# Kernel optimization log

Measured on AMD Instinct MI355X. Metric: run time of the kernel, lower is better.

## Reference

```python
import jax, jax.numpy as jnp
import numpy as np

ALPHA = 0.2  # LeakyReLU negative slope
N, IN_DIM, OUT_DIM = 8192, 128, 64


def setup_inputs() -> dict:
    key = jax.random.key(0)
    k1, k2, k3, k4 = jax.random.split(key, 4)
    x = jax.random.normal(k1, (N, IN_DIM), dtype=jnp.float32)
    adj = jax.random.randint(k2, (N, N), 0, 2, dtype=jnp.int32)
    W = jax.random.normal(k3, (IN_DIM, OUT_DIM), dtype=jnp.float32) * 0.1
    a = jax.random.normal(k4, (2 * OUT_DIM, 1), dtype=jnp.float32) * 0.1
    return {"x": x, "adj": adj, "W": W, "a": a}


def reference(x, adj, W, a):
    # h = x @ W : [N, out]
    h = x @ W
    # e_ij = LeakyReLU(a^T [h_i || h_j]) computed as broadcast sum of the
    # two halves of the attention vector (avoids materializing [N,N,2*out]).
    a_src = a[:OUT_DIM, 0]   # [out]
    a_dst = a[OUT_DIM:, 0]   # [out]
    e = (h @ a_src)[:, None] + (h @ a_dst)[None, :]      # [N, N]
    e = jnp.where(e > 0, e, ALPHA * e)                    # LeakyReLU
    # mask non-edges, row-softmax
    e = jnp.where(adj > 0, e, jnp.float32(-9e15))
    attn = jax.nn.softmax(e, axis=-1)                     # [N, N]
    out = attn @ h                                        # [N, out]
    # concat=True -> ELU nonlinearity
    return jax.nn.elu(out)
```

## Files before the change

kernel.cpp:

```cpp
#include <hip/hip_runtime.h>
#include <hip/hip_bf16.h>
#include <cstdint>
#include <cstddef>

#define N_NODES 8192
#define IN_DIM  128
#define OUT_DIM 64
#define LRELU_ALPHA 0.2f
#define S_SLICES 4
#define LOG2E 1.44269504f

using f32x16 = __attribute__((ext_vector_type(16))) float;
using bf16x8 = __attribute__((ext_vector_type(8))) short;

typedef const __attribute__((address_space(1))) int* gas_ptr;
typedef __attribute__((address_space(3))) int* las_ptr;

static __device__ __forceinline__ unsigned short f2bf(float x) {
    union { float f; unsigned u; } v; v.f = x;
    unsigned r = v.u + 0x7FFFu + ((v.u >> 16) & 1u);
    return (unsigned short)(r >> 16);
}

__global__ __launch_bounds__(256) void gat_prep(
    const float* __restrict__ x, const float* __restrict__ W,
    const float* __restrict__ a,
    float* __restrict__ svec, float* __restrict__ dvec,
    unsigned short* __restrict__ hpack)
{
    __shared__ float shA[4][8][64];
    const int tid = threadIdx.x;
    const int w   = tid >> 6;
    const int f   = tid & 63;
    const int i0  = blockIdx.x * 8;

    float acc[8];
#pragma unroll
    for (int r = 0; r < 8; ++r) acc[r] = 0.f;

    const int k0 = w * 32;
#pragma unroll 2
    for (int k = k0; k < k0 + 32; k += 4) {
        const float w0 = W[(k + 0) * OUT_DIM + f];
        const float w1 = W[(k + 1) * OUT_DIM + f];
        const float w2 = W[(k + 2) * OUT_DIM + f];
        const float w3 = W[(k + 3) * OUT_DIM + f];
#pragma unroll
        for (int r = 0; r < 8; ++r) {
            const float4 xv = *reinterpret_cast<const float4*>(
                x + (size_t)(i0 + r) * IN_DIM + k);
            acc[r] = fmaf(xv.x, w0, acc[r]);
            acc[r] = fmaf(xv.y, w1, acc[r]);
            acc[r] = fmaf(xv.z, w2, acc[r]);
            acc[r] = fmaf(xv.w, w3, acc[r]);
        }
    }
#pragma unroll
    for (int r = 0; r < 8; ++r) shA[w][r][f] = acc[r];
    __syncthreads();

    if (w == 0) {
        union { unsigned short us[8]; int4 v; } pk;
#pragma unroll
        for (int r = 0; r < 8; ++r) {
            const float hv = shA[0][r][f] + shA[1][r][f] + shA[2][r][f] + shA[3][r][f];
            pk.us[r] = f2bf(hv);
        }
        const int jb    = i0 >> 4;
        const int jhalf = (i0 >> 3) & 1;
        const int fb    = f >> 5;
        const int lidx  = (f & 31) + 32 * jhalf;
        *reinterpret_cast<int4*>(hpack + ((size_t)(jb * 2 + fb) * 64 + lidx) * 8) = pk.v;
    } else if (w == 1) {
        const float asrc = a[f];
#pragma unroll
        for (int r = 0; r < 8; ++r) {
            const float hv = shA[0][r][f] + shA[1][r][f] + shA[2][r][f] + shA[3][r][f];
            float sv = hv * asrc;
#pragma unroll
            for (int off = 32; off >= 1; off >>= 1) sv += __shfl_xor(sv, off);
            if (f == 0) svec[i0 + r] = sv * LOG2E;
        }
    } else if (w == 2) {
        const float adst = a[OUT_DIM + f];
#pragma unroll
        for (int r = 0; r < 8; ++r) {
            const float hv = shA[0][r][f] + shA[1][r][f] + shA[2][r][f] + shA[3][r][f];
            float dv = hv * adst;
#pragma unroll
            for (int off = 32; off >= 1; off >>= 1) dv += __shfl_xor(dv, off);
            if (f == 0) dvec[i0 + r] = dv * LOG2E;
        }
    }
}

__global__ __launch_bounds__(256, 4) void gat_main(
    const int* __restrict__ adj,
    const float* __restrict__ svec, const float* __restrict__ dvec,
    const unsigned short* __restrict__ hpack,
    float* __restrict__ pO, float* __restrict__ pDen)
{
    union SH {
        int tiles[2][32 * 128];
        struct { float red[4][32][64]; float redden[4][32]; } r;
    };
    __shared__ SH sh;

    const int tid = threadIdx.x;
    const int w   = tid >> 6;
    const int l   = tid & 63;
    const int rb  = blockIdx.x;
    const int sl  = blockIdx.y;
    const int row = l & 31;
    const int kh  = l >> 5;
    const int i0  = rb * 32;
    const int jwin = sl * 2048;

    const float s_i = svec[i0 + row];
    asm volatile("" :: "v"(s_i));
    const bf16x8* hp = reinterpret_cast<const bf16x8*>(hpack);

    auto stage = [&](int buf, int ss) {
        const int jt0 = jwin + ss * 128;
#pragma unroll
        for (int q = 0; q < 4; ++q) {
            const int r0   = (w * 4 + q) * 2;
            const int lrow = r0 + (l >> 5);
            const int cp   = l & 31;
            const int cg   = cp ^ (lrow & 7);
            const int* gsrc = adj + (size_t)(i0 + lrow) * N_NODES + jt0 + cg * 4;
            int* ldst = &sh.tiles[buf][r0 * 128];
            __builtin_amdgcn_global_load_lds((gas_ptr)gsrc, (las_ptr)ldst, 16, 0, 0);
        }
    };

    f32x16 acc0, acc1;
#pragma unroll
    for (int r = 0; r < 16; ++r) { acc0[r] = 0.f; acc1[r] = 0.f; }
    float den = 0.f;

    stage(0, 0);
    stage(1, 1);

    const int swz = row & 7;
    for (int s = 0; s < 16; ++s) {
        const int buf = s & 1;
        const int jt0 = jwin + s * 128;
        const int jg  = jt0 + w * 32;
        const int jb  = jg >> 4;

        const bf16x8 b00 = hp[(jb * 2 + 0) * 64 + l];
        const bf16x8 b01 = hp[(jb * 2 + 1) * 64 + l];
        const bf16x8 b10 = hp[(jb * 2 + 2) * 64 + l];
        const bf16x8 b11 = hp[(jb * 2 + 3) * 64 + l];
        const int j0 = jg + kh * 8;
        const float4 dA0 = *reinterpret_cast<const float4*>(dvec + j0);
        const float4 dA1 = *reinterpret_cast<const float4*>(dvec + j0 + 4);
        const float4 dB0 = *reinterpret_cast<const float4*>(dvec + j0 + 16);
        const float4 dB1 = *reinterpret_cast<const float4*>(dvec + j0 + 20);

        asm volatile("s_waitcnt vmcnt(12)" ::: "memory");
        __builtin_amdgcn_s_barrier();

        const int* tb = &sh.tiles[buf][0];
        const int c00 = w * 8 + kh * 2;
        const int c10 = w * 8 + 4 + kh * 2;
        const int4 A00 = *reinterpret_cast<const int4*>(&tb[row * 128 + ((c00    ) ^ swz) * 4]);
        const int4 A01 = *reinterpret_cast<const int4*>(&tb[row * 128 + ((c00 + 1) ^ swz) * 4]);
        const int4 A10 = *reinterpret_cast<const int4*>(&tb[row * 128 + ((c10    ) ^ swz) * 4]);
        const int4 A11 = *reinterpret_cast<const int4*>(&tb[row * 128 + ((c10 + 1) ^ swz) * 4]);
        asm volatile("s_waitcnt lgkmcnt(0)" ::: "memory");
        __builtin_amdgcn_s_barrier();

        if (s + 2 < 16) stage(buf, s + 2);

        const float dd0[8] = {dA0.x, dA0.y, dA0.z, dA0.w, dA1.x, dA1.y, dA1.z, dA1.w};
        const int   ia0[8] = {A00.x, A00.y, A00.z, A00.w, A01.x, A01.y, A01.z, A01.w};
        const float dd1[8] = {dB0.x, dB0.y, dB0.z, dB0.w, dB1.x, dB1.y, dB1.z, dB1.w};
        const int   ia1[8] = {A10.x, A10.y, A10.z, A10.w, A11.x, A11.y, A11.z, A11.w};

        bf16x8 af0, af1;
#pragma unroll
        for (int e = 0; e < 8; ++e) {
            float ev = s_i + dd0[e];
            ev = fmaxf(ev, LRELU_ALPHA * ev);
            float pv = __builtin_amdgcn_exp2f(ev);
            pv = (ia0[e] > 0) ? pv : 0.f;
            union { float f; unsigned u; } pu; pu.f = pv;
            pu.u &= 0xFFFF0000u;
            den += pu.f;
            af0[e] = (short)(pu.u >> 16);
        }
#pragma unroll
        for (int e = 0; e < 8; ++e) {
            float ev = s_i + dd1[e];
            ev = fmaxf(ev, LRELU_ALPHA * ev);
            float pv = __builtin_amdgcn_exp2f(ev);
            pv = (ia1[e] > 0) ? pv : 0.f;
            union { float f; unsigned u; } pu; pu.f = pv;
            pu.u &= 0xFFFF0000u;
            den += pu.f;
            af1[e] = (short)(pu.u >> 16);
        }
        acc0 = __builtin_amdgcn_mfma_f32_32x32x16_bf16(af0, b00, acc0, 0, 0, 0);
        acc1 = __builtin_amdgcn_mfma_f32_32x32x16_bf16(af0, b01, acc1, 0, 0, 0);
        acc0 = __builtin_amdgcn_mfma_f32_32x32x16_bf16(af1, b10, acc0, 0, 0, 0);
        acc1 = __builtin_amdgcn_mfma_f32_32x32x16_bf16(af1, b11, acc1, 0, 0, 0);
    }

    __syncthreads();

#pragma unroll
    for (int r = 0; r < 16; ++r) {
        const int orow = (r & 3) + 8 * (r >> 2) + 4 * kh;
        sh.r.red[w][orow][row]      = acc0[r];
        sh.r.red[w][orow][32 + row] = acc1[r];
    }
    const float dtot = den + __shfl_xor(den, 32);
    if (l < 32) sh.r.redden[w][l] = dtot;
    __syncthreads();

    float* po = pO + ((size_t)rb * S_SLICES + sl) * 2048;
    const float* rf = &sh.r.red[0][0][0];
    for (int e = tid; e < 2048; e += 256)
        po[e] = rf[e] + rf[2048 + e] + rf[4096 + e] + rf[6144 + e];
    if (tid < 32) {
        pDen[((size_t)rb * S_SLICES + sl) * 32 + tid] =
            sh.r.redden[0][tid] + sh.r.redden[1][tid] +
            sh.r.redden[2][tid] + sh.r.redden[3][tid];
    }
}

__global__ __launch_bounds__(256) void gat_final(
    const float* __restrict__ pO, const float* __restrict__ pDen,
    float* __restrict__ out)
{
    const int idx = blockIdx.x * 256 + threadIdx.x;
    const int i = idx >> 6;
    const int f = idx & 63;
    const int rb = i >> 5;
    const int r  = i & 31;
    const float* po = pO + (size_t)rb * S_SLICES * 2048 + r * 64 + f;
    const float v = po[0] + po[2048] + po[4096] + po[6144];
    const float* pd = pDen + (size_t)rb * S_SLICES * 32 + r;
    const float dsum = pd[0] + pd[32] + pd[64] + pd[96];
    const float o = v / dsum;
    out[idx] = (o > 0.f) ? o : expm1f(o);
}

extern "C" void kernel_launch(void* const* d_in, const int* in_sizes, int n_in,
                              void* d_out, int out_size, void* d_ws, size_t ws_size,
                              hipStream_t stream)
{
    const float* x   = (const float*)d_in[0];
    const int*   adj = (const int*)d_in[1];
    const float* W   = (const float*)d_in[2];
    const float* a   = (const float*)d_in[3];
    float* out = (float*)d_out;

    float* svec = (float*)d_ws;
    float* dvec = svec + N_NODES;
    unsigned short* hpack = (unsigned short*)(dvec + N_NODES);
    float* pO = (float*)(hpack + (size_t)N_NODES * OUT_DIM);
    float* pDen = pO + (size_t)256 * S_SLICES * 2048;

    gat_prep<<<N_NODES / 8, 256, 0, stream>>>(x, W, a, svec, dvec, hpack);
    gat_main<<<dim3(256, S_SLICES), 256, 0, stream>>>(adj, svec, dvec, hpack, pO, pDen);
    gat_final<<<(N_NODES * OUT_DIM) / 256, 256, 0, stream>>>(pO, pDen, out);
}
```

Baseline: 70.71 us.

## Drop column slicing, widen blocks to 8 waves, fuse final normalization into main kernel

Each block now processes a full 32-row strip across all 8192 columns with 512 threads instead of splitting columns across 4 blocks. This lets the softmax normalization and ELU be done in-block, removing the partial-sum buffers and the separate final kernel launch. Tiles are widened to 256 columns per step. The trade-off is fewer blocks (one per CU), which may reduce memory-level parallelism for streaming the adjacency matrix.

```diff
diff --git a/kernel.cpp b/kernel.cpp
--- a/kernel.cpp
+++ b/kernel.cpp
@@ -7,8 +7,8 @@
 #define IN_DIM  128
 #define OUT_DIM 64
 #define LRELU_ALPHA 0.2f
-#define S_SLICES 4
 #define LOG2E 1.44269504f
+#define NSTEP 32
 
 using f32x16 = __attribute__((ext_vector_type(16))) float;
 using bf16x8 = __attribute__((ext_vector_type(8))) short;
@@ -94,15 +94,15 @@
     }
 }
 
-__global__ __launch_bounds__(256, 4) void gat_main(
+__global__ __launch_bounds__(512, 2) void gat_main(
     const int* __restrict__ adj,
     const float* __restrict__ svec, const float* __restrict__ dvec,
     const unsigned short* __restrict__ hpack,
-    float* __restrict__ pO, float* __restrict__ pDen)
+    float* __restrict__ out)
 {
     union SH {
-        int tiles[2][32 * 128];
-        struct { float red[4][32][64]; float redden[4][32]; } r;
+        int tiles[2][32 * 256];
+        struct { float red[8][32][64]; float redden[8][32]; } r;
     };
     __shared__ SH sh;
 
@@ -110,26 +110,22 @@
     const int w   = tid >> 6;
     const int l   = tid & 63;
     const int rb  = blockIdx.x;
-    const int sl  = blockIdx.y;
     const int row = l & 31;
     const int kh  = l >> 5;
     const int i0  = rb * 32;
-    const int jwin = sl * 2048;
 
     const float s_i = svec[i0 + row];
     asm volatile("" :: "v"(s_i));
     const bf16x8* hp = reinterpret_cast<const bf16x8*>(hpack);
 
     auto stage = [&](int buf, int ss) {
-        const int jt0 = jwin + ss * 128;
+        const int jt0 = ss * 256;
 #pragma unroll
         for (int q = 0; q < 4; ++q) {
-            const int r0   = (w * 4 + q) * 2;
-            const int lrow = r0 + (l >> 5);
-            const int cp   = l & 31;
-            const int cg   = cp ^ (lrow & 7);
-            const int* gsrc = adj + (size_t)(i0 + lrow) * N_NODES + jt0 + cg * 4;
-            int* ldst = &sh.tiles[buf][r0 * 128];
+            const int r0 = w * 4 + q;
+            const int cg = l ^ (r0 & 7);
+            const int* gsrc = adj + (size_t)(i0 + r0) * N_NODES + jt0 + cg * 4;
+            int* ldst = &sh.tiles[buf][r0 * 256];
             __builtin_amdgcn_global_load_lds((gas_ptr)gsrc, (las_ptr)ldst, 16, 0, 0);
         }
     };
@@ -143,10 +139,9 @@
     stage(1, 1);
 
     const int swz = row & 7;
-    for (int s = 0; s < 16; ++s) {
+    for (int s = 0; s < NSTEP; ++s) {
         const int buf = s & 1;
-        const int jt0 = jwin + s * 128;
-        const int jg  = jt0 + w * 32;
+        const int jg  = s * 256 + w * 32;
         const int jb  = jg >> 4;
 
         const bf16x8 b00 = hp[(jb * 2 + 0) * 64 + l];
@@ -159,20 +154,21 @@
         const float4 dB0 = *reinterpret_cast<const float4*>(dvec + j0 + 16);
         const float4 dB1 = *reinterpret_cast<const float4*>(dvec + j0 + 20);
 
-        asm volatile("s_waitcnt vmcnt(12)" ::: "memory");
+        if (s == NSTEP - 1) asm volatile("s_waitcnt vmcnt(8)"  ::: "memory");
+        else                asm volatile("s_waitcnt vmcnt(12)" ::: "memory");
         __builtin_amdgcn_s_barrier();
 
         const int* tb = &sh.tiles[buf][0];
         const int c00 = w * 8 + kh * 2;
         const int c10 = w * 8 + 4 + kh * 2;
-        const int4 A00 = *reinterpret_cast<const int4*>(&tb[row * 128 + ((c00    ) ^ swz) * 4]);
-        const int4 A01 = *reinterpret_cast<const int4*>(&tb[row * 128 + ((c00 + 1) ^ swz) * 4]);
-        const int4 A10 = *reinterpret_cast<const int4*>(&tb[row * 128 + ((c10    ) ^ swz) * 4]);
-        const int4 A11 = *reinterpret_cast<const int4*>(&tb[row * 128 + ((c10 + 1) ^ swz) * 4]);
+        const int4 A00 = *reinterpret_cast<const int4*>(&tb[row * 256 + ((c00    ) ^ swz) * 4]);
+        const int4 A01 = *reinterpret_cast<const int4*>(&tb[row * 256 + ((c00 + 1) ^ swz) * 4]);
+        const int4 A10 = *reinterpret_cast<const int4*>(&tb[row * 256 + ((c10    ) ^ swz) * 4]);
+        const int4 A11 = *reinterpret_cast<const int4*>(&tb[row * 256 + ((c10 + 1) ^ swz) * 4]);
         asm volatile("s_waitcnt lgkmcnt(0)" ::: "memory");
         __builtin_amdgcn_s_barrier();
 
-        if (s + 2 < 16) stage(buf, s + 2);
+        if (s + 2 < NSTEP) stage(buf, s + 2);
 
         const float dd0[8] = {dA0.x, dA0.y, dA0.z, dA0.w, dA1.x, dA1.y, dA1.z, dA1.w};
         const int   ia0[8] = {A00.x, A00.y, A00.z, A00.w, A01.x, A01.y, A01.z, A01.w};
@@ -220,32 +216,17 @@
     if (l < 32) sh.r.redden[w][l] = dtot;
     __syncthreads();
 
-    float* po = pO + ((size_t)rb * S_SLICES + sl) * 2048;
-    const float* rf = &sh.r.red[0][0][0];
-    for (int e = tid; e < 2048; e += 256)
-        po[e] = rf[e] + rf[2048 + e] + rf[4096 + e] + rf[6144 + e];
-    if (tid < 32) {
-        pDen[((size_t)rb * S_SLICES + sl) * 32 + tid] =
-            sh.r.redden[0][tid] + sh.r.redden[1][tid] +
-            sh.r.redden[2][tid] + sh.r.redden[3][tid];
-    }
-}
-
-__global__ __launch_bounds__(256) void gat_final(
-    const float* __restrict__ pO, const float* __restrict__ pDen,
-    float* __restrict__ out)
-{
-    const int idx = blockIdx.x * 256 + threadIdx.x;
-    const int i = idx >> 6;
-    const int f = idx & 63;
-    const int rb = i >> 5;
-    const int r  = i & 31;
-    const float* po = pO + (size_t)rb * S_SLICES * 2048 + r * 64 + f;
-    const float v = po[0] + po[2048] + po[4096] + po[6144];
-    const float* pd = pDen + (size_t)rb * S_SLICES * 32 + r;
-    const float dsum = pd[0] + pd[32] + pd[64] + pd[96];
-    const float o = v / dsum;
-    out[idx] = (o > 0.f) ? o : expm1f(o);
+    for (int e = tid; e < 32 * 64; e += 512) {
+        const int orow = e >> 6;
+        float v = 0.f, dsum = 0.f;
+#pragma unroll
+        for (int ww = 0; ww < 8; ++ww) {
+            v    += sh.r.red[ww][orow][e & 63];
+            dsum += sh.r.redden[ww][orow];
+        }
+        const float o = v / dsum;
+        out[(size_t)(i0 + orow) * OUT_DIM + (e & 63)] = (o > 0.f) ? o : expm1f(o);
+    }
 }
 
 extern "C" void kernel_launch(void* const* d_in, const int* in_sizes, int n_in,
@@ -261,10 +242,7 @@
     float* svec = (float*)d_ws;
     float* dvec = svec + N_NODES;
     unsigned short* hpack = (unsigned short*)(dvec + N_NODES);
-    float* pO = (float*)(hpack + (size_t)N_NODES * OUT_DIM);
-    float* pDen = pO + (size_t)256 * S_SLICES * 2048;
 
     gat_prep<<<N_NODES / 8, 256, 0, stream>>>(x, W, a, svec, dvec, hpack);
-    gat_main<<<dim3(256, S_SLICES), 256, 0, stream>>>(adj, svec, dvec, hpack, pO, pDen);
-    gat_final<<<(N_NODES * OUT_DIM) / 256, 256, 0, stream>>>(pO, pDen, out);
-}
+    gat_main<<<256, 512, 0, stream>>>(adj, svec, dvec, hpack, out);
+}
```

New measurement: 73.47 us. +3.9%, slower.

## Give each wave a private adjacency column window and drop per-step block barriers

Applied to the files above, without the earlier changes.

Each wave now streams its own contiguous 512-column window of the adjacency tile into a private LDS double buffer. This removes the two s_barrier calls per pipeline step. The hpack/dvec operand loads are also prefetched one step ahead into registers, with vmcnt waits tuned to that ordering. The aim is to cut synchronisation stalls and hide global-load latency, at the cost of more live registers, which could hurt occupancy under launch_bounds(256,4).

```diff
diff --git a/kernel.cpp b/kernel.cpp
--- a/kernel.cpp
+++ b/kernel.cpp
@@ -9,6 +9,7 @@
 #define LRELU_ALPHA 0.2f
 #define S_SLICES 4
 #define LOG2E 1.44269504f
+#define NSTEP 16
 
 using f32x16 = __attribute__((ext_vector_type(16))) float;
 using bf16x8 = __attribute__((ext_vector_type(8))) short;
@@ -101,7 +102,7 @@
     float* __restrict__ pO, float* __restrict__ pDen)
 {
     union SH {
-        int tiles[2][32 * 128];
+        int tiles[4][2][1024];
         struct { float red[4][32][64]; float redden[4][32]; } r;
     };
     __shared__ SH sh;
@@ -114,24 +115,44 @@
     const int row = l & 31;
     const int kh  = l >> 5;
     const int i0  = rb * 32;
-    const int jwin = sl * 2048;
+    const int jwv = sl * 2048 + w * 512;
 
     const float s_i = svec[i0 + row];
     asm volatile("" :: "v"(s_i));
     const bf16x8* hp = reinterpret_cast<const bf16x8*>(hpack);
 
+    const int lrow8 = l >> 3;
+    const int lu    = l & 7;
+
     auto stage = [&](int buf, int ss) {
-        const int jt0 = jwin + ss * 128;
+        const int jt = jwv + ss * 32;
 #pragma unroll
         for (int q = 0; q < 4; ++q) {
-            const int r0   = (w * 4 + q) * 2;
-            const int lrow = r0 + (l >> 5);
-            const int cp   = l & 31;
-            const int cg   = cp ^ (lrow & 7);
-            const int* gsrc = adj + (size_t)(i0 + lrow) * N_NODES + jt0 + cg * 4;
-            int* ldst = &sh.tiles[buf][r0 * 128];
-            __builtin_amdgcn_global_load_lds((gas_ptr)gsrc, (las_ptr)ldst, 16, 0, 0);
-        }
+            const int rq = q * 8 + lrow8;
+            const int cu = lu ^ (rq & 7);
+            const int* gs = adj + (size_t)(i0 + rq) * N_NODES + jt + cu * 4;
+            __builtin_amdgcn_global_load_lds((gas_ptr)gs,
+                (las_ptr)&sh.tiles[w][buf][q * 256], 16, 0, 0);
+        }
+    };
+
+    bf16x8 b00, b01, b10, b11, nb00, nb01, nb10, nb11;
+    float4 dA0, dA1, dB0, dB1, nA0, nA1, nB0, nB1;
+
+    auto loadP = [&](int ss,
+                     bf16x8& x00, bf16x8& x01, bf16x8& x10, bf16x8& x11,
+                     float4& y0, float4& y1, float4& y2, float4& y3) {
+        const int jg = jwv + ss * 32;
+        const int jb = jg >> 4;
+        x00 = hp[(jb * 2 + 0) * 64 + l];
+        x01 = hp[(jb * 2 + 1) * 64 + l];
+        x10 = hp[(jb * 2 + 2) * 64 + l];
+        x11 = hp[(jb * 2 + 3) * 64 + l];
+        const int j0 = jg + kh * 8;
+        y0 = *reinterpret_cast<const float4*>(dvec + j0);
+        y1 = *reinterpret_cast<const float4*>(dvec + j0 + 4);
+        y2 = *reinterpret_cast<const float4*>(dvec + j0 + 16);
+        y3 = *reinterpret_cast<const float4*>(dvec + j0 + 20);
     };
 
     f32x16 acc0, acc1;
@@ -140,39 +161,37 @@
     float den = 0.f;
 
     stage(0, 0);
+    asm volatile("" ::: "memory");
+    loadP(0, b00, b01, b10, b11, dA0, dA1, dB0, dB1);
+    asm volatile("" ::: "memory");
     stage(1, 1);
-
-    const int swz = row & 7;
-    for (int s = 0; s < 16; ++s) {
-        const int buf = s & 1;
-        const int jt0 = jwin + s * 128;
-        const int jg  = jt0 + w * 32;
-        const int jb  = jg >> 4;
-
-        const bf16x8 b00 = hp[(jb * 2 + 0) * 64 + l];
-        const bf16x8 b01 = hp[(jb * 2 + 1) * 64 + l];
-        const bf16x8 b10 = hp[(jb * 2 + 2) * 64 + l];
-        const bf16x8 b11 = hp[(jb * 2 + 3) * 64 + l];
-        const int j0 = jg + kh * 8;
-        const float4 dA0 = *reinterpret_cast<const float4*>(dvec + j0);
-        const float4 dA1 = *reinterpret_cast<const float4*>(dvec + j0 + 4);
-        const float4 dB0 = *reinterpret_cast<const float4*>(dvec + j0 + 16);
-        const float4 dB1 = *reinterpret_cast<const float4*>(dvec + j0 + 20);
-
-        asm volatile("s_waitcnt vmcnt(12)" ::: "memory");
-        __builtin_amdgcn_s_barrier();
-
-        const int* tb = &sh.tiles[buf][0];
-        const int c00 = w * 8 + kh * 2;
-        const int c10 = w * 8 + 4 + kh * 2;
-        const int4 A00 = *reinterpret_cast<const int4*>(&tb[row * 128 + ((c00    ) ^ swz) * 4]);
-        const int4 A01 = *reinterpret_cast<const int4*>(&tb[row * 128 + ((c00 + 1) ^ swz) * 4]);
-        const int4 A10 = *reinterpret_cast<const int4*>(&tb[row * 128 + ((c10    ) ^ swz) * 4]);
-        const int4 A11 = *reinterpret_cast<const int4*>(&tb[row * 128 + ((c10 + 1) ^ swz) * 4]);
+    asm volatile("" ::: "memory");
+
+    const int swz  = row & 7;
+    const int base = row * 32;
+
+#pragma unroll 1
+    for (int s = 0; s < NSTEP; ++s) {
+        if (s < NSTEP - 1) asm volatile("s_waitcnt vmcnt(4)" ::: "memory");
+        else               asm volatile("s_waitcnt vmcnt(0)" ::: "memory");
+
+        const int* tb = &sh.tiles[w][s & 1][0];
+        const int c0 = kh * 2;
+        const int c1 = 4 + kh * 2;
+        const int4 A00 = *reinterpret_cast<const int4*>(&tb[base + ((c0    ) ^ swz) * 4]);
+        const int4 A01 = *reinterpret_cast<const int4*>(&tb[base + ((c0 + 1) ^ swz) * 4]);
+        const int4 A10 = *reinterpret_cast<const int4*>(&tb[base + ((c1    ) ^ swz) * 4]);
+        const int4 A11 = *reinterpret_cast<const int4*>(&tb[base + ((c1 + 1) ^ swz) * 4]);
         asm volatile("s_waitcnt lgkmcnt(0)" ::: "memory");
-        __builtin_amdgcn_s_barrier();
-
-        if (s + 2 < 16) stage(buf, s + 2);
+
+        if (s + 1 < NSTEP) {
+            loadP(s + 1, nb00, nb01, nb10, nb11, nA0, nA1, nB0, nB1);
+            asm volatile("" ::: "memory");
+        }
+        if (s + 2 < NSTEP) {
+            stage(s & 1, s + 2);
+            asm volatile("" ::: "memory");
+        }
 
         const float dd0[8] = {dA0.x, dA0.y, dA0.z, dA0.w, dA1.x, dA1.y, dA1.z, dA1.w};
         const int   ia0[8] = {A00.x, A00.y, A00.z, A00.w, A01.x, A01.y, A01.z, A01.w};
@@ -206,6 +225,11 @@
         acc1 = __builtin_amdgcn_mfma_f32_32x32x16_bf16(af0, b01, acc1, 0, 0, 0);
         acc0 = __builtin_amdgcn_mfma_f32_32x32x16_bf16(af1, b10, acc0, 0, 0, 0);
         acc1 = __builtin_amdgcn_mfma_f32_32x32x16_bf16(af1, b11, acc1, 0, 0, 0);
+
+        if (s + 1 < NSTEP) {
+            b00 = nb00; b01 = nb01; b10 = nb10; b11 = nb11;
+            dA0 = nA0;  dA1 = nA1;  dB0 = nB0;  dB1 = nB1;
+        }
     }
 
     __syncthreads();
```

Result: slower. 96.21 us (+36.1%).

## Compress adjacency tiles to ballot bitmasks in LDS with register-prefetched loads

Applied to the files above, without the earlier changes.

The old path copied 32x128 int adjacency tiles into LDS with global_load_lds and read four int4 values per lane. It is replaced by coalesced per-lane global loads into 32 registers for a 256-column super-tile. Each wave then uses __ballot to pack those values into 64-bit bitmasks, which are stored in a small double-buffered LDS array. The main loop reads one u64 mask per lane and extracts per-element bits, so LDS traffic and the barrier count drop. The cost is 32 live registers of prefetch per lane, which may pressure occupancy at launch_bounds(256,4), plus 32 ballots per stage.

```diff
diff --git a/kernel.cpp b/kernel.cpp
--- a/kernel.cpp
+++ b/kernel.cpp
@@ -9,12 +9,11 @@
 #define LRELU_ALPHA 0.2f
 #define S_SLICES 4
 #define LOG2E 1.44269504f
+#define NSUP 8
 
 using f32x16 = __attribute__((ext_vector_type(16))) float;
 using bf16x8 = __attribute__((ext_vector_type(8))) short;
-
-typedef const __attribute__((address_space(1))) int* gas_ptr;
-typedef __attribute__((address_space(3))) int* las_ptr;
+typedef unsigned long long u64;
 
 static __device__ __forceinline__ unsigned short f2bf(float x) {
     union { float f; unsigned u; } v; v.f = x;
@@ -101,7 +100,7 @@
     float* __restrict__ pO, float* __restrict__ pDen)
 {
     union SH {
-        int tiles[2][32 * 128];
+        u64 bits[2][128];
         struct { float red[4][32][64]; float redden[4][32]; } r;
     };
     __shared__ SH sh;
@@ -117,21 +116,28 @@
     const int jwin = sl * 2048;
 
     const float s_i = svec[i0 + row];
-    asm volatile("" :: "v"(s_i));
     const bf16x8* hp = reinterpret_cast<const bf16x8*>(hpack);
 
-    auto stage = [&](int buf, int ss) {
-        const int jt0 = jwin + ss * 128;
-#pragma unroll
-        for (int q = 0; q < 4; ++q) {
-            const int r0   = (w * 4 + q) * 2;
-            const int lrow = r0 + (l >> 5);
-            const int cp   = l & 31;
-            const int cg   = cp ^ (lrow & 7);
-            const int* gsrc = adj + (size_t)(i0 + lrow) * N_NODES + jt0 + cg * 4;
-            int* ldst = &sh.tiles[buf][r0 * 128];
-            __builtin_amdgcn_global_load_lds((gas_ptr)gsrc, (las_ptr)ldst, 16, 0, 0);
-        }
+    int av[32];
+
+    auto loads = [&](int S) {
+        const int j0s = jwin + S * 256;
+#pragma unroll
+        for (int r8 = 0; r8 < 8; ++r8)
+#pragma unroll
+            for (int g = 0; g < 4; ++g)
+                av[r8 * 4 + g] =
+                    adj[(size_t)(i0 + w * 8 + r8) * N_NODES + j0s + g * 64 + l];
+    };
+
+    auto ballots_and_write = [&](int plane) {
+        unsigned keepLo = 0, keepHi = 0;
+#pragma unroll
+        for (int m = 0; m < 32; ++m) {
+            const u64 b = __ballot(av[m] != 0);
+            if (l == m) { keepLo = (unsigned)b; keepHi = (unsigned)(b >> 32); }
+        }
+        if (l < 32) sh.bits[plane][w * 32 + l] = ((u64)keepHi << 32) | keepLo;
     };
 
     f32x16 acc0, acc1;
@@ -139,76 +145,77 @@
     for (int r = 0; r < 16; ++r) { acc0[r] = 0.f; acc1[r] = 0.f; }
     float den = 0.f;
 
-    stage(0, 0);
-    stage(1, 1);
-
-    const int swz = row & 7;
-    for (int s = 0; s < 16; ++s) {
-        const int buf = s & 1;
-        const int jt0 = jwin + s * 128;
-        const int jg  = jt0 + w * 32;
-        const int jb  = jg >> 4;
-
-        const bf16x8 b00 = hp[(jb * 2 + 0) * 64 + l];
-        const bf16x8 b01 = hp[(jb * 2 + 1) * 64 + l];
-        const bf16x8 b10 = hp[(jb * 2 + 2) * 64 + l];
-        const bf16x8 b11 = hp[(jb * 2 + 3) * 64 + l];
-        const int j0 = jg + kh * 8;
-        const float4 dA0 = *reinterpret_cast<const float4*>(dvec + j0);
-        const float4 dA1 = *reinterpret_cast<const float4*>(dvec + j0 + 4);
-        const float4 dB0 = *reinterpret_cast<const float4*>(dvec + j0 + 16);
-        const float4 dB1 = *reinterpret_cast<const float4*>(dvec + j0 + 20);
-
-        asm volatile("s_waitcnt vmcnt(12)" ::: "memory");
-        __builtin_amdgcn_s_barrier();
-
-        const int* tb = &sh.tiles[buf][0];
-        const int c00 = w * 8 + kh * 2;
-        const int c10 = w * 8 + 4 + kh * 2;
-        const int4 A00 = *reinterpret_cast<const int4*>(&tb[row * 128 + ((c00    ) ^ swz) * 4]);
-        const int4 A01 = *reinterpret_cast<const int4*>(&tb[row * 128 + ((c00 + 1) ^ swz) * 4]);
-        const int4 A10 = *reinterpret_cast<const int4*>(&tb[row * 128 + ((c10    ) ^ swz) * 4]);
-        const int4 A11 = *reinterpret_cast<const int4*>(&tb[row * 128 + ((c10 + 1) ^ swz) * 4]);
+    loads(0);
+    ballots_and_write(0);
+    asm volatile("s_waitcnt lgkmcnt(0)" ::: "memory");
+    __builtin_amdgcn_s_barrier();
+    asm volatile("" ::: "memory");
+
+#pragma unroll 1
+    for (int S = 0; S < NSUP; ++S) {
+        const int plane = S & 1;
+        const int j0s   = jwin + S * 256;
+
+        const u64 wv = sh.bits[plane][row * 4 + w];
+
+        if (S + 1 < NSUP) loads(S + 1);
+
+#pragma unroll
+        for (int ti = 0; ti < 2; ++ti) {
+            const unsigned b32 = ti ? (unsigned)(wv >> 32) : (unsigned)wv;
+            const int jg = j0s + (w * 2 + ti) * 32;
+            const int jb = jg >> 4;
+            const bf16x8 b00 = hp[(jb * 2 + 0) * 64 + l];
+            const bf16x8 b01 = hp[(jb * 2 + 1) * 64 + l];
+            const bf16x8 b10 = hp[(jb * 2 + 2) * 64 + l];
+            const bf16x8 b11 = hp[(jb * 2 + 3) * 64 + l];
+            const int j0 = jg + kh * 8;
+            const float4 dA0 = *reinterpret_cast<const float4*>(dvec + j0);
+            const float4 dA1 = *reinterpret_cast<const float4*>(dvec + j0 + 4);
+            const float4 dB0 = *reinterpret_cast<const float4*>(dvec + j0 + 16);
+            const float4 dB1 = *reinterpret_cast<const float4*>(dvec + j0 + 20);
+
+            const unsigned mq0 = b32 >> (kh * 8);
+            const unsigned mq1 = b32 >> (16 + kh * 8);
+
+            const float dd0[8] = {dA0.x, dA0.y, dA0.z, dA0.w, dA1.x, dA1.y, dA1.z, dA1.w};
+            const float dd1[8] = {dB0.x, dB0.y, dB0.z, dB0.w, dB1.x, dB1.y, dB1.z, dB1.w};
+
+            bf16x8 af0, af1;
+#pragma unroll
+            for (int e = 0; e < 8; ++e) {
+                float ev = s_i + dd0[e];
+                ev = fmaxf(ev, LRELU_ALPHA * ev);
+                float pv = __builtin_amdgcn_exp2f(ev);
+                pv = ((mq0 >> e) & 1u) ? pv : 0.f;
+                union { float f; unsigned u; } pu; pu.f = pv;
+                pu.u &= 0xFFFF0000u;
+                den += pu.f;
+                af0[e] = (short)(pu.u >> 16);
+            }
+#pragma unroll
+            for (int e = 0; e < 8; ++e) {
+                float ev = s_i + dd1[e];
+                ev = fmaxf(ev, LRELU_ALPHA * ev);
+                float pv = __builtin_amdgcn_exp2f(ev);
+                pv = ((mq1 >> e) & 1u) ? pv : 0.f;
+                union { float f; unsigned u; } pu; pu.f = pv;
+                pu.u &= 0xFFFF0000u;
+                den += pu.f;
+                af1[e] = (short)(pu.u >> 16);
+            }
+            acc0 = __builtin_amdgcn_mfma_f32_32x32x16_bf16(af0, b00, acc0, 0, 0, 0);
+            acc1 = __builtin_amdgcn_mfma_f32_32x32x16_bf16(af0, b01, acc1, 0, 0, 0);
+            acc0 = __builtin_amdgcn_mfma_f32_32x32x16_bf16(af1, b10, acc0, 0, 0, 0);
+            acc1 = __builtin_amdgcn_mfma_f32_32x32x16_bf16(af1, b11, acc1, 0, 0, 0);
+        }
+
+        if (S + 1 < NSUP) ballots_and_write(plane ^ 1);
+
         asm volatile("s_waitcnt lgkmcnt(0)" ::: "memory");
         __builtin_amdgcn_s_barrier();
-
-        if (s + 2 < 16) stage(buf, s + 2);
-
-        const float dd0[8] = {dA0.x, dA0.y, dA0.z, dA0.w, dA1.x, dA1.y, dA1.z, dA1.w};
-        const int   ia0[8] = {A00.x, A00.y, A00.z, A00.w, A01.x, A01.y, A01.z, A01.w};
-        const float dd1[8] = {dB0.x, dB0.y, dB0.z, dB0.w, dB1.x, dB1.y, dB1.z, dB1.w};
-        const int   ia1[8] = {A10.x, A10.y, A10.z, A10.w, A11.x, A11.y, A11.z, A11.w};
-
-        bf16x8 af0, af1;
-#pragma unroll
-        for (int e = 0; e < 8; ++e) {
-            float ev = s_i + dd0[e];
-            ev = fmaxf(ev, LRELU_ALPHA * ev);
-            float pv = __builtin_amdgcn_exp2f(ev);
-            pv = (ia0[e] > 0) ? pv : 0.f;
-            union { float f; unsigned u; } pu; pu.f = pv;
-            pu.u &= 0xFFFF0000u;
-            den += pu.f;
-            af0[e] = (short)(pu.u >> 16);
-        }
-#pragma unroll
-        for (int e = 0; e < 8; ++e) {
-            float ev = s_i + dd1[e];
-            ev = fmaxf(ev, LRELU_ALPHA * ev);
-            float pv = __builtin_amdgcn_exp2f(ev);
-            pv = (ia1[e] > 0) ? pv : 0.f;
-            union { float f; unsigned u; } pu; pu.f = pv;
-            pu.u &= 0xFFFF0000u;
-            den += pu.f;
-            af1[e] = (short)(pu.u >> 16);
-        }
-        acc0 = __builtin_amdgcn_mfma_f32_32x32x16_bf16(af0, b00, acc0, 0, 0, 0);
-        acc1 = __builtin_amdgcn_mfma_f32_32x32x16_bf16(af0, b01, acc1, 0, 0, 0);
-        acc0 = __builtin_amdgcn_mfma_f32_32x32x16_bf16(af1, b10, acc0, 0, 0, 0);
-        acc1 = __builtin_amdgcn_mfma_f32_32x32x16_bf16(af1, b11, acc1, 0, 0, 0);
-    }
-
-    __syncthreads();
+        asm volatile("" ::: "memory");
+    }
 
 #pragma unroll
     for (int r = 0; r < 16; ++r) {
```

Measured after the change: 92.05 us. +30.2%, slower.
